# Kernel tuning notes

Hardware: AMD Instinct MI355X
Metric: run time of the kernel (lower is better)

Reference implementation:

```python
import jax, jax.numpy as jnp
import numpy as np

B, S, D_MODEL, N_HEADS = 4, 2048, 1024, 16
HEAD_DIM = D_MODEL // N_HEADS  # 64; used only for the softmax scale, as in the source


def setup_inputs() -> dict:
    key = jax.random.key(0)
    kq, kk, kv, kw = jax.random.split(key, 4)
    q = jax.random.normal(kq, (B, S, D_MODEL), dtype=jnp.float32)
    k = jax.random.normal(kk, (B, S, D_MODEL), dtype=jnp.float32)
    v = jax.random.normal(kv, (B, S, D_MODEL), dtype=jnp.float32)
    # out_proj: nn.Linear(d_model, d_model, bias=False) -> weight [out, in]
    W_out = jax.random.normal(kw, (D_MODEL, D_MODEL), dtype=jnp.float32) * (1.0 / np.sqrt(D_MODEL))
    return {"q": q, "k": k, "v": v, "W_out": W_out}


def reference(q, k, v, W_out):
    scale = 1.0 / jnp.sqrt(jnp.float32(HEAD_DIM))
    # scores: [B, Sq, Sk] -- full quadratic score matrix, as in the source
    scores = jnp.einsum("bqd,bkd->bqk", q, k) * scale
    attn = jax.nn.softmax(scores, axis=-1)
    out = jnp.einsum("bqk,bkd->bqd", attn, v)
    # torch Linear: y = x @ W^T
    return jnp.einsum("bsd,ed->bse", out, W_out)
```

## Files before the change

### kernel.cpp

```cpp
#include <hip/hip_runtime.h>
#include <hip/hip_fp16.h>
#include <stdint.h>

typedef _Float16 h16;
typedef _Float16 h16x8 __attribute__((ext_vector_type(8)));
typedef float f32x4 __attribute__((ext_vector_type(4)));

#define BB 4
#define SS 2048
#define DD 1024

#define EPI_H16 0
#define EPI_EXP 1
#define EPI_DIV 2

__device__ __forceinline__ void gload16(const void* g, void* l) {
    __builtin_amdgcn_global_load_lds(
        (const __attribute__((address_space(1))) uint32_t*)g,
        (__attribute__((address_space(3))) uint32_t*)l, 16, 0, 0);
}

__global__ __launch_bounds__(256) void cvt_qk(
    const float* __restrict__ q, const float* __restrict__ k,
    h16* __restrict__ qh, h16* __restrict__ kh) {
    int b = blockIdx.x;
    const float* src; h16* dst; float sc = 1.0f;
    if (b < 1024)      { src = q; dst = qh; sc = 0.125f; }
    else               { src = k; dst = kh; b -= 1024; }
    size_t base = (size_t)b * 2048 + threadIdx.x;
    float4 a[8];
#pragma unroll
    for (int i = 0; i < 8; ++i) a[i] = ((const float4*)src)[base + (size_t)i * 256];
#pragma unroll
    for (int i = 0; i < 8; ++i) {
        union { int2 i2; h16 h[4]; } u;
        u.h[0] = (h16)(a[i].x * sc); u.h[1] = (h16)(a[i].y * sc);
        u.h[2] = (h16)(a[i].z * sc); u.h[3] = (h16)(a[i].w * sc);
        ((int2*)dst)[base + (size_t)i * 256] = u.i2;
    }
}

__global__ __launch_bounds__(512, 2) void gemm1_fused(
    const h16* __restrict__ A, const h16* __restrict__ B, h16* __restrict__ C,
    const float* __restrict__ v, const float* __restrict__ w,
    h16* __restrict__ vh, h16* __restrict__ wh)
{
    constexpr int ABYTES = 256 * 128;
    constexpr int BBYTES = 256 * 128;
    constexpr int BUFB   = ABYTES + BBYTES;
    __shared__ __align__(1024) char lds[2 * BUFB];

    const int tid = threadIdx.x;

    if (blockIdx.x < 64) {
        const int lane = blockIdx.x * 512 + tid;
#pragma unroll 4
        for (int i = 0; i < 64; ++i) {
            size_t g = (size_t)i * 32768 + lane;
            float4 a = ((const float4*)v)[g];
            union { int2 i2; h16 h[4]; } u;
            u.h[0] = (h16)a.x; u.h[1] = (h16)a.y; u.h[2] = (h16)a.z; u.h[3] = (h16)a.w;
            ((int2*)vh)[g] = u.i2;
        }
#pragma unroll
        for (int i = 0; i < 8; ++i) {
            size_t g = (size_t)i * 32768 + lane;
            float4 a = ((const float4*)w)[g];
            union { int2 i2; h16 h[4]; } u;
            u.h[0] = (h16)a.x; u.h[1] = (h16)a.y; u.h[2] = (h16)a.z; u.h[3] = (h16)a.w;
            ((int2*)wh)[g] = u.i2;
        }
        return;
    }

    const int gid = blockIdx.x - 64;
    const int wgid = (gid & 7) * 32 + (gid >> 3);
    const int bb  = wgid / 64;
    const int rem = wgid % 64;
    const int tm = rem / 8, tn = rem % 8;
    const int row0 = tm * 256, col0 = tn * 256;

    const h16* Ab = A + (long long)bb * ((long long)SS * DD);
    const h16* Bb = B + (long long)bb * ((long long)SS * DD);

    const int lane = tid & 63, wid = tid >> 6;
    const int wm = wid >> 2, wn = wid & 3;
    const int frow = lane & 15, kq = lane >> 4;

    const int NT = DD >> 6;

    f32x4 acc[8][4];
#pragma unroll
    for (int m = 0; m < 8; ++m)
#pragma unroll
        for (int n = 0; n < 4; ++n) acc[m][n] = (f32x4){0.f, 0.f, 0.f, 0.f};

    char* l0 = (char*)lds;

    auto STAGE_B = [&](int kt, int buf) {
#pragma unroll
        for (int i = 0; i < 4; ++i) {
            int d = i * 512 + tid;
            int s = d & 7, r = d >> 3;
            int gg = s ^ (r & 7);
            gload16(Bb + (size_t)(col0 + r) * DD + kt + gg * 8,
                    l0 + buf * BUFB + ABYTES + (r * 8 + s) * 16);
        }
    };
    auto STAGE_AH = [&](int kt, int buf, int mh) {
#pragma unroll
        for (int i = 0; i < 2; ++i) {
            int d = i * 512 + tid;
            int s = d & 7, hr = d >> 3;
            int r = ((hr & ~63) << 1) + mh * 64 + (hr & 63);
            int gg = s ^ (r & 7);
            gload16(Ab + (size_t)(row0 + r) * DD + kt + gg * 8,
                    l0 + buf * BUFB + (r * 8 + s) * 16);
        }
    };
    auto READ_A = [&](int buf, int mh, h16x8 (&af)[4][2]) {
#pragma unroll
        for (int mm = 0; mm < 4; ++mm)
#pragma unroll
            for (int ks = 0; ks < 2; ++ks) {
                int r = wm * 128 + (mh * 4 + mm) * 16 + frow;
                int s = (ks * 4 + kq) ^ (r & 7);
                af[mm][ks] = *(const h16x8*)(l0 + buf * BUFB + (r * 8 + s) * 16);
            }
    };
    auto READ_B = [&](int buf, h16x8 (&bf)[4][2]) {
#pragma unroll
        for (int nn = 0; nn < 4; ++nn)
#pragma unroll
            for (int ks = 0; ks < 2; ++ks) {
                int r = wn * 64 + nn * 16 + frow;
                int s = (ks * 4 + kq) ^ (r & 7);
                bf[nn][ks] = *(const h16x8*)(l0 + buf * BUFB + ABYTES + (r * 8 + s) * 16);
            }
    };
    auto MFMA_H = [&](int mh, h16x8 (&af)[4][2], h16x8 (&bf)[4][2]) {
        __builtin_amdgcn_s_setprio(1);
#pragma unroll
        for (int ks = 0; ks < 2; ++ks)
#pragma unroll
            for (int mm = 0; mm < 4; ++mm)
#pragma unroll
                for (int nn = 0; nn < 4; ++nn)
                    acc[mh * 4 + mm][nn] =
                        __builtin_amdgcn_mfma_f32_16x16x32_f16(
                            af[mm][ks], bf[nn][ks], acc[mh * 4 + mm][nn], 0, 0, 0);
        __builtin_amdgcn_s_setprio(0);
    };

    STAGE_B(0, 0); STAGE_AH(0, 0, 0); STAGE_AH(0, 0, 1);
    asm volatile("s_waitcnt vmcnt(2)" ::: "memory");
    __builtin_amdgcn_s_barrier();

    h16x8 af[4][2], bf[4][2];

    for (int G = 0; G < NT; ++G) {
        const int buf = G & 1;
        const int kt1 = (G + 1) << 6;
        if (G + 1 < NT) {
            STAGE_B(kt1, buf ^ 1);
            STAGE_AH(kt1, buf ^ 1, 0);
            STAGE_AH(kt1, buf ^ 1, 1);
        }
        READ_A(buf, 0, af);
        READ_B(buf, bf);
        MFMA_H(0, af, bf);
        if (G + 1 < NT) asm volatile("s_waitcnt vmcnt(8)" ::: "memory");
        else            asm volatile("s_waitcnt vmcnt(0)" ::: "memory");
        __builtin_amdgcn_s_barrier();
        READ_A(buf, 1, af);
        MFMA_H(1, af, bf);
        if (G + 1 >= NT) break;
        asm volatile("s_waitcnt vmcnt(2)" ::: "memory");
        __builtin_amdgcn_s_barrier();
    }

    h16* Cb = C + (long long)bb * ((long long)SS * SS);
    const int erow = row0 + wm * 128 + (lane >> 4) * 4;
    const int ecol = col0 + wn * 64 + (lane & 15);
#pragma unroll
    for (int m = 0; m < 8; ++m)
#pragma unroll
        for (int n = 0; n < 4; ++n)
#pragma unroll
            for (int j = 0; j < 4; ++j)
                Cb[(size_t)(erow + m * 16 + j) * SS + (ecol + n * 16)] =
                    (h16)__expf(acc[m][n][j] - 16.0f);
}

template<int EPI>
__global__ __launch_bounds__(256, 2) void gemm2p_sm(
    const h16* __restrict__ A, const h16* __restrict__ B, void* __restrict__ Cv,
    int lda, int ldb, int ldc, int K, int tilesN, int tilesMN,
    long long aBatch, long long bBatch, long long cBatch, const float* __restrict__ rsum)
{
    constexpr int ABYTES = 128 * 128;
    constexpr int BBYTES = 128 * 128;
    constexpr int BUFB   = ABYTES + BBYTES;

    __shared__ __align__(1024) char lds[2 * BUFB];

    const int tid = threadIdx.x;
    const int nwg = gridDim.x;
    const int bid = blockIdx.x;
    const int wgid = (bid & 7) * (nwg >> 3) + (bid >> 3);
    const int bb  = wgid / tilesMN;
    const int rem = wgid % tilesMN;
    const int tm = rem / tilesN, tn = rem % tilesN;
    const int row0 = tm * 128, col0 = tn * 128;

    const h16* Ab = A + (long long)bb * aBatch;
    const h16* Bb = B + (long long)bb * bBatch;

    const int lane = tid & 63, wid = tid >> 6;
    const int wm = wid >> 1, wn = wid & 1;
    const int frow = lane & 15, kq = lane >> 4;

    const int NT = K >> 6;

    f32x4 acc[4][4];
#pragma unroll
    for (int m = 0; m < 4; ++m)
#pragma unroll
        for (int n = 0; n < 4; ++n) acc[m][n] = (f32x4){0.f, 0.f, 0.f, 0.f};

    char* l0 = (char*)lds;

    auto STAGE_B = [&](int kt, int buf) {
#pragma unroll
        for (int i = 0; i < 4; ++i) {
            int d = i * 256 + tid;
            int s = d & 7, r = d >> 3;
            int gg = s ^ (r & 7);
            gload16(Bb + (size_t)(col0 + r) * ldb + kt + gg * 8,
                    l0 + buf * BUFB + ABYTES + (r * 8 + s) * 16);
        }
    };
    auto STAGE_AH = [&](int kt, int buf, int mh) {
#pragma unroll
        for (int i = 0; i < 2; ++i) {
            int d = i * 256 + tid;
            int s = d & 7, hr = d >> 3;
            int r = ((hr & ~31) << 1) + mh * 32 + (hr & 31);
            int gg = s ^ (r & 7);
            gload16(Ab + (size_t)(row0 + r) * lda + kt + gg * 8,
                    l0 + buf * BUFB + (r * 8 + s) * 16);
        }
    };
    auto READ_A = [&](int buf, int mh, h16x8 (&af)[2][2]) {
#pragma unroll
        for (int mm = 0; mm < 2; ++mm)
#pragma unroll
            for (int ks = 0; ks < 2; ++ks) {
                int r = wm * 64 + (mh * 2 + mm) * 16 + frow;
                int s = (ks * 4 + kq) ^ (r & 7);
                af[mm][ks] = *(const h16x8*)(l0 + buf * BUFB + (r * 8 + s) * 16);
            }
    };
    auto READ_B = [&](int buf, h16x8 (&bf)[4][2]) {
#pragma unroll
        for (int nn = 0; nn < 4; ++nn)
#pragma unroll
            for (int ks = 0; ks < 2; ++ks) {
                int r = wn * 64 + nn * 16 + frow;
                int s = (ks * 4 + kq) ^ (r & 7);
                bf[nn][ks] = *(const h16x8*)(l0 + buf * BUFB + ABYTES + (r * 8 + s) * 16);
            }
    };
    auto MFMA_H = [&](int mh, h16x8 (&af)[2][2], h16x8 (&bf)[4][2]) {
        __builtin_amdgcn_s_setprio(1);
#pragma unroll
        for (int ks = 0; ks < 2; ++ks)
#pragma unroll
            for (int mm = 0; mm < 2; ++mm)
#pragma unroll
                for (int nn = 0; nn < 4; ++nn)
                    acc[mh * 2 + mm][nn] =
                        __builtin_amdgcn_mfma_f32_16x16x32_f16(
                            af[mm][ks], bf[nn][ks], acc[mh * 2 + mm][nn], 0, 0, 0);
        __builtin_amdgcn_s_setprio(0);
    };

    STAGE_B(0, 0); STAGE_AH(0, 0, 0); STAGE_AH(0, 0, 1);
    asm volatile("s_waitcnt vmcnt(2)" ::: "memory");
    __builtin_amdgcn_s_barrier();

    h16x8 af[2][2], bf[4][2];

    for (int G = 0; G < NT; ++G) {
        const int buf = G & 1;
        const int kt1 = (G + 1) << 6;
        if (G + 1 < NT) {
            STAGE_B(kt1, buf ^ 1);
            STAGE_AH(kt1, buf ^ 1, 0);
            STAGE_AH(kt1, buf ^ 1, 1);
        }
        READ_A(buf, 0, af);
        READ_B(buf, bf);
        MFMA_H(0, af, bf);
        if (G + 1 < NT) asm volatile("s_waitcnt vmcnt(8)" ::: "memory");
        else            asm volatile("s_waitcnt vmcnt(0)" ::: "memory");
        __builtin_amdgcn_s_barrier();
        READ_A(buf, 1, af);
        MFMA_H(1, af, bf);
        if (G + 1 >= NT) break;
        asm volatile("s_waitcnt vmcnt(2)" ::: "memory");
        __builtin_amdgcn_s_barrier();
    }

    const int erow = row0 + wm * 64 + (lane >> 4) * 4;
    const int ecol = col0 + wn * 64 + (lane & 15);
#pragma unroll
    for (int m = 0; m < 4; ++m)
#pragma unroll
        for (int n = 0; n < 4; ++n)
#pragma unroll
            for (int j = 0; j < 4; ++j) {
                int row = erow + m * 16 + j, col = ecol + n * 16;
                float vv = acc[m][n][j];
                if constexpr (EPI == EPI_DIV) {
                    float* C = (float*)Cv + (long long)bb * cBatch;
                    C[(size_t)row * ldc + col] = vv * rsum[bb * SS + row];
                } else if constexpr (EPI == EPI_EXP) {
                    h16* C = (h16*)Cv + (long long)bb * cBatch;
                    C[(size_t)row * ldc + col] = (h16)__expf(vv - 16.0f);
                } else {
                    h16* C = (h16*)Cv + (long long)bb * cBatch;
                    C[(size_t)row * ldc + col] = (h16)vv;
                }
            }
}

__global__ __launch_bounds__(256) void rowsumE(const h16* __restrict__ sc,
                                               float* __restrict__ rsum) {
    const int row = blockIdx.x;
    const h16* rp = sc + (size_t)row * 2048;
    union { int4 i4; h16 h[8]; } u;
    u.i4 = ((const int4*)rp)[threadIdx.x];
    float s = 0.f;
#pragma unroll
    for (int j = 0; j < 8; ++j) s += (float)u.h[j];
#pragma unroll
    for (int off = 32; off; off >>= 1) s += __shfl_xor(s, off);
    __shared__ float ws[4];
    const int lane = threadIdx.x & 63, wid = threadIdx.x >> 6;
    if (lane == 0) ws[wid] = s;
    __syncthreads();
    if (threadIdx.x == 0)
        rsum[row] = 1.0f / (ws[0] + ws[1] + ws[2] + ws[3]);
}

extern "C" void kernel_launch(void* const* d_in, const int* in_sizes, int n_in,
                              void* d_out, int out_size, void* d_ws, size_t ws_size,
                              hipStream_t stream) {
    (void)in_sizes; (void)n_in; (void)out_size; (void)ws_size;
    const float* q = (const float*)d_in[0];
    const float* k = (const float*)d_in[1];
    const float* v = (const float*)d_in[2];
    const float* w = (const float*)d_in[3];
    float* out = (float*)d_out;

    const size_t QKV = (size_t)BB * SS * DD;
    h16* qh = (h16*)d_ws;
    h16* kh = qh + QKV;
    h16* vh = kh + QKV;
    h16* wh = vh + QKV;
    h16* sc = wh + (size_t)DD * DD;
    float* rsum = (float*)(sc + (size_t)BB * SS * SS);

    cvt_qk<<<2048, 256, 0, stream>>>(q, k, qh, kh);

    gemm1_fused<<<320, 512, 0, stream>>>(qh, kh, sc, v, w, vh, wh);

    rowsumE<<<BB * SS, 256, 0, stream>>>(sc, rsum);

    h16* vpT = qh;
    gemm2p_sm<EPI_H16><<<512, 256, 0, stream>>>(
        wh, vh, (void*)vpT, DD, DD, BB * SS, DD, 64, 512,
        0LL, 0LL, 0LL, nullptr);

    gemm2p_sm<EPI_DIV><<<512, 256, 0, stream>>>(
        sc, vpT, (void*)out, SS, BB * SS, DD, SS, 8, 128,
        (long long)SS * SS, (long long)SS, (long long)SS * DD, rsum);
}
```

Baseline: 134.5 us.

## Fuse softmax row sums into QK GEMM epilogue and interleave V/W conversion

The separate rowsumE kernel is removed. Each GEMM1 tile now reduces its exp values across lanes with shuffles and atomically adds partial row sums into a rowsum buffer, which cvt_qk zero-initialises. The V and W fp32-to-fp16 conversion moves out of 64 dedicated blocks and into the GEMM1 main loop, with one float4 per thread per k-iteration. This removes a kernel launch and a full re-read of the score matrix, and it balances conversion work across all blocks. In exchange it adds atomics, a division in the final epilogue, and extra global traffic inside the GEMM pipeline that could disturb the vmcnt-based wait accounting.

```diff
diff --git a/kernel.cpp b/kernel.cpp
--- a/kernel.cpp
+++ b/kernel.cpp
@@ -11,7 +11,6 @@
 #define DD 1024
 
 #define EPI_H16 0
-#define EPI_EXP 1
 #define EPI_DIV 2
 
 __device__ __forceinline__ void gload16(const void* g, void* l) {
@@ -22,7 +21,11 @@
 
 __global__ __launch_bounds__(256) void cvt_qk(
     const float* __restrict__ q, const float* __restrict__ k,
-    h16* __restrict__ qh, h16* __restrict__ kh) {
+    h16* __restrict__ qh, h16* __restrict__ kh, float* __restrict__ rowsum) {
+    if (blockIdx.x == 0) {
+#pragma unroll
+        for (int i = 0; i < 32; ++i) rowsum[threadIdx.x + i * 256] = 0.f;
+    }
     int b = blockIdx.x;
     const float* src; h16* dst; float sc = 1.0f;
     if (b < 1024)      { src = q; dst = qh; sc = 0.125f; }
@@ -40,40 +43,25 @@
     }
 }
 
-__global__ __launch_bounds__(512, 2) void gemm1_fused(
+__device__ __forceinline__ void cvt_store(h16* dst, size_t g, float4 a) {
+    union { int2 i2; h16 h[4]; } u;
+    u.h[0] = (h16)a.x; u.h[1] = (h16)a.y; u.h[2] = (h16)a.z; u.h[3] = (h16)a.w;
+    ((int2*)dst)[g] = u.i2;
+}
+
+__global__ __launch_bounds__(512, 2) void gemm1f(
     const h16* __restrict__ A, const h16* __restrict__ B, h16* __restrict__ C,
     const float* __restrict__ v, const float* __restrict__ w,
-    h16* __restrict__ vh, h16* __restrict__ wh)
+    h16* __restrict__ vh, h16* __restrict__ wh, float* __restrict__ rowsum)
 {
     constexpr int ABYTES = 256 * 128;
-    constexpr int BBYTES = 256 * 128;
-    constexpr int BUFB   = ABYTES + BBYTES;
+    constexpr int BUFB   = 2 * ABYTES;
     __shared__ __align__(1024) char lds[2 * BUFB];
 
     const int tid = threadIdx.x;
-
-    if (blockIdx.x < 64) {
-        const int lane = blockIdx.x * 512 + tid;
-#pragma unroll 4
-        for (int i = 0; i < 64; ++i) {
-            size_t g = (size_t)i * 32768 + lane;
-            float4 a = ((const float4*)v)[g];
-            union { int2 i2; h16 h[4]; } u;
-            u.h[0] = (h16)a.x; u.h[1] = (h16)a.y; u.h[2] = (h16)a.z; u.h[3] = (h16)a.w;
-            ((int2*)vh)[g] = u.i2;
-        }
-#pragma unroll
-        for (int i = 0; i < 8; ++i) {
-            size_t g = (size_t)i * 32768 + lane;
-            float4 a = ((const float4*)w)[g];
-            union { int2 i2; h16 h[4]; } u;
-            u.h[0] = (h16)a.x; u.h[1] = (h16)a.y; u.h[2] = (h16)a.z; u.h[3] = (h16)a.w;
-            ((int2*)wh)[g] = u.i2;
-        }
-        return;
-    }
-
-    const int gid = blockIdx.x - 64;
+    const int gid = blockIdx.x;
+    const size_t tidg = (size_t)gid * 512 + tid;
+
     const int wgid = (gid & 7) * 32 + (gid >> 3);
     const int bb  = wgid / 64;
     const int rem = wgid % 64;
@@ -152,15 +140,25 @@
         __builtin_amdgcn_s_setprio(0);
     };
 
+    {
+        float4 w0 = ((const float4*)w)[tidg];
+        float4 w1 = ((const float4*)w)[131072 + tidg];
+        cvt_store(wh, tidg, w0);
+        cvt_store(wh, 131072 + tidg, w1);
+    }
     STAGE_B(0, 0); STAGE_AH(0, 0, 0); STAGE_AH(0, 0, 1);
     asm volatile("s_waitcnt vmcnt(2)" ::: "memory");
     __builtin_amdgcn_s_barrier();
 
     h16x8 af[4][2], bf[4][2];
+    float4 vbuf;
 
     for (int G = 0; G < NT; ++G) {
         const int buf = G & 1;
         const int kt1 = (G + 1) << 6;
+        float4 vnew = ((const float4*)v)[(size_t)G * 131072 + tidg];
+        if (G > 0) cvt_store(vh, (size_t)(G - 1) * 131072 + tidg, vbuf);
+        vbuf = vnew;
         if (G + 1 < NT) {
             STAGE_B(kt1, buf ^ 1);
             STAGE_AH(kt1, buf ^ 1, 0);
@@ -178,25 +176,37 @@
         asm volatile("s_waitcnt vmcnt(2)" ::: "memory");
         __builtin_amdgcn_s_barrier();
     }
+    cvt_store(vh, (size_t)(NT - 1) * 131072 + tidg, vbuf);
 
     h16* Cb = C + (long long)bb * ((long long)SS * SS);
+    float* rs = rowsum + bb * SS;
     const int erow = row0 + wm * 128 + (lane >> 4) * 4;
     const int ecol = col0 + wn * 64 + (lane & 15);
 #pragma unroll
     for (int m = 0; m < 8; ++m)
 #pragma unroll
-        for (int n = 0; n < 4; ++n)
-#pragma unroll
-            for (int j = 0; j < 4; ++j)
-                Cb[(size_t)(erow + m * 16 + j) * SS + (ecol + n * 16)] =
-                    (h16)__expf(acc[m][n][j] - 16.0f);
+        for (int j = 0; j < 4; ++j) {
+            const int row = erow + m * 16 + j;
+            float p = 0.f;
+#pragma unroll
+            for (int n = 0; n < 4; ++n) {
+                float e = __expf(acc[m][n][j] - 16.0f);
+                Cb[(size_t)row * SS + (ecol + n * 16)] = (h16)e;
+                p += e;
+            }
+            p += __shfl_xor(p, 1);
+            p += __shfl_xor(p, 2);
+            p += __shfl_xor(p, 4);
+            p += __shfl_xor(p, 8);
+            if ((lane & 15) == 0) atomicAdd(&rs[row], p);
+        }
 }
 
 template<int EPI>
 __global__ __launch_bounds__(256, 2) void gemm2p_sm(
     const h16* __restrict__ A, const h16* __restrict__ B, void* __restrict__ Cv,
     int lda, int ldb, int ldc, int K, int tilesN, int tilesMN,
-    long long aBatch, long long bBatch, long long cBatch, const float* __restrict__ rsum)
+    long long aBatch, long long bBatch, long long cBatch, const float* __restrict__ rowsum)
 {
     constexpr int ABYTES = 128 * 128;
     constexpr int BBYTES = 128 * 128;
@@ -324,34 +334,12 @@
                 float vv = acc[m][n][j];
                 if constexpr (EPI == EPI_DIV) {
                     float* C = (float*)Cv + (long long)bb * cBatch;
-                    C[(size_t)row * ldc + col] = vv * rsum[bb * SS + row];
-                } else if constexpr (EPI == EPI_EXP) {
-                    h16* C = (h16*)Cv + (long long)bb * cBatch;
-                    C[(size_t)row * ldc + col] = (h16)__expf(vv - 16.0f);
+                    C[(size_t)row * ldc + col] = vv / rowsum[bb * SS + row];
                 } else {
                     h16* C = (h16*)Cv + (long long)bb * cBatch;
                     C[(size_t)row * ldc + col] = (h16)vv;
                 }
             }
-}
-
-__global__ __launch_bounds__(256) void rowsumE(const h16* __restrict__ sc,
-                                               float* __restrict__ rsum) {
-    const int row = blockIdx.x;
-    const h16* rp = sc + (size_t)row * 2048;
-    union { int4 i4; h16 h[8]; } u;
-    u.i4 = ((const int4*)rp)[threadIdx.x];
-    float s = 0.f;
-#pragma unroll
-    for (int j = 0; j < 8; ++j) s += (float)u.h[j];
-#pragma unroll
-    for (int off = 32; off; off >>= 1) s += __shfl_xor(s, off);
-    __shared__ float ws[4];
-    const int lane = threadIdx.x & 63, wid = threadIdx.x >> 6;
-    if (lane == 0) ws[wid] = s;
-    __syncthreads();
-    if (threadIdx.x == 0)
-        rsum[row] = 1.0f / (ws[0] + ws[1] + ws[2] + ws[3]);
 }
 
 extern "C" void kernel_launch(void* const* d_in, const int* in_sizes, int n_in,
@@ -370,13 +358,11 @@
     h16* vh = kh + QKV;
     h16* wh = vh + QKV;
     h16* sc = wh + (size_t)DD * DD;
-    float* rsum = (float*)(sc + (size_t)BB * SS * SS);
-
-    cvt_qk<<<2048, 256, 0, stream>>>(q, k, qh, kh);
-
-    gemm1_fused<<<320, 512, 0, stream>>>(qh, kh, sc, v, w, vh, wh);
-
-    rowsumE<<<BB * SS, 256, 0, stream>>>(sc, rsum);
+    float* rowsum = (float*)(sc + (size_t)BB * SS * SS);
+
+    cvt_qk<<<2048, 256, 0, stream>>>(q, k, qh, kh, rowsum);
+
+    gemm1f<<<256, 512, 0, stream>>>(qh, kh, sc, v, w, vh, wh, rowsum);
 
     h16* vpT = qh;
     gemm2p_sm<EPI_H16><<<512, 256, 0, stream>>>(
@@ -385,5 +371,5 @@
 
     gemm2p_sm<EPI_DIV><<<512, 256, 0, stream>>>(
         sc, vpT, (void*)out, SS, BB * SS, DD, SS, 8, 128,
-        (long long)SS * SS, (long long)SS, (long long)SS * DD, rsum);
-}
+        (long long)SS * SS, (long long)SS, (long long)SS * DD, rowsum);
+}
```

Measured after the change: 131.1 us. -2.5%, faster.
